# Kernel tuning notes

Measured on AMD Instinct MI355X. Metric: run time of the kernel, lower is better.

Reference implementation:

```python
import jax, jax.numpy as jnp
import numpy as np

H = 12      # num_heads
DIN = 768   # input_embedding_dim
D = 64      # embedding_dim (per head)
N, T = 4, 1024


def setup_inputs() -> dict:
    key = jax.random.key(0)
    ks = jax.random.split(key, 6)
    s_in = 1.0 / np.sqrt(DIN)
    s_hd = 1.0 / np.sqrt(H * D)
    x = jax.random.normal(ks[0], (N, T, DIN), dtype=jnp.float32)
    # Per-head bias-free projections stacked over heads: [H, DIN, D]
    Wq = jax.random.uniform(ks[1], (H, DIN, D), jnp.float32, -s_in, s_in)
    Wk = jax.random.uniform(ks[2], (H, DIN, D), jnp.float32, -s_in, s_in)
    Wv = jax.random.uniform(ks[3], (H, DIN, D), jnp.float32, -s_in, s_in)
    # Output projection: Linear(H*D -> D) with bias
    Wo = jax.random.uniform(ks[4], (H * D, D), jnp.float32, -s_hd, s_hd)
    bo = jax.random.uniform(ks[5], (D,), jnp.float32, -s_hd, s_hd)
    return {"x": x, "Wq": Wq, "Wk": Wk, "Wv": Wv, "Wo": Wo, "bo": bo}


def reference(x, Wq, Wk, Wv, Wo, bo):
    n, t, _ = x.shape
    # Batched per-head projections (all heads at once): [N,H,T,D]
    q = jnp.einsum('ntd,hde->nhte', x, Wq)
    k = jnp.einsum('ntd,hde->nhte', x, Wk)
    v = jnp.einsum('ntd,hde->nhte', x, Wv)
    # Raw scores (note: original applies NO 1/sqrt(D) scaling): [N,H,T,T]
    att = jnp.einsum('nhte,nhse->nhts', q, k)
    # Faithful to torch: tril zeros the upper triangle, then ALL zeros -> -inf
    causal = jnp.tril(jnp.ones((t, t), dtype=bool))
    att = jnp.where(causal, att, 0.0)
    att = jnp.where(att == 0.0, -jnp.inf, att)
    attn = jax.nn.softmax(att, axis=-1)  # [N,H,T,T]
    # Weighted values, then concat heads along feature dim (head-major order)
    o = jnp.einsum('nhts,nhse->nhte', attn, v)          # [N,H,T,D]
    o = jnp.transpose(o, (0, 2, 1, 3)).reshape(n, t, -1)  # [N,T,H*D]
    out = o @ Wo + bo  # [N,T,D]
    return out, attn
```

## Files before the change

kernel.cpp:

```cpp
#include <hip/hip_runtime.h>
#include <hip/hip_bf16.h>

typedef __hip_bfloat16 bf16;
typedef __attribute__((ext_vector_type(8))) short bf16x8;
typedef __attribute__((ext_vector_type(4))) float f32x4;

constexpr int NB  = 4;
constexpr int NH  = 12;
constexpr int SEQ = 1024;
constexpr int HD  = 64;
constexpr int DM  = 768;
constexpr int LDA = 40;

__device__ __forceinline__ bf16x8 ld8(const bf16* p){ return *(const bf16x8*)p; }
__device__ __forceinline__ f32x4 mfma16(bf16x8 a, bf16x8 b, f32x4 c){
  return __builtin_amdgcn_mfma_f32_16x16x32_bf16(a, b, c, 0, 0, 0);
}
union U8 { bf16x8 v; bf16 h[8]; };

__global__ __launch_bounds__(256) void wprep(const float* __restrict__ Wq, const float* __restrict__ Wk,
                      const float* __restrict__ Wv, const float* __restrict__ Wo,
                      bf16* __restrict__ WqTh, bf16* __restrict__ WqTl,
                      bf16* __restrict__ WkTh, bf16* __restrict__ WkTl,
                      bf16* __restrict__ WvT,  bf16* __restrict__ WoT){
  __shared__ float sT[64][65];
  const int tid = threadIdx.x;
  const int dt = blockIdx.x, y = blockIdx.y;
  const float* src; bf16* dh; bf16* dl = nullptr;
  if (y < 36){
    int z = y / 12, h = y % 12;
    src = (z==0 ? Wq : z==1 ? Wk : Wv) + (size_t)h*DM*HD;
    dh  = (z==0 ? WqTh : z==1 ? WkTh : WvT) + (size_t)h*HD*DM;
    if (z==0) dl = WqTl + (size_t)h*HD*DM;
    if (z==1) dl = WkTl + (size_t)h*HD*DM;
  } else { src = Wo; dh = WoT; }

  {
    int r = tid >> 2, c = (tid & 3) * 16;
    const float* sp = src + ((size_t)(dt*64 + r))*HD + c;
    f32x4 v0 = *(const f32x4*)sp, v1 = *(const f32x4*)(sp+4),
          v2 = *(const f32x4*)(sp+8), v3 = *(const f32x4*)(sp+12);
    #pragma unroll
    for (int j = 0; j < 4; j++){
      sT[r][c+j] = v0[j]; sT[r][c+4+j] = v1[j]; sT[r][c+8+j] = v2[j]; sT[r][c+12+j] = v3[j];
    }
  }
  __syncthreads();
  {
    int e = tid >> 2, co = (tid & 3) * 16;
    U8 uh0, ul0, uh1, ul1;
    #pragma unroll
    for (int j = 0; j < 8; j++){
      float v = sT[co + j][e];
      bf16 hi = __float2bfloat16(v);
      uh0.h[j] = hi; ul0.h[j] = __float2bfloat16(v - __bfloat162float(hi));
    }
    #pragma unroll
    for (int j = 0; j < 8; j++){
      float v = sT[co + 8 + j][e];
      bf16 hi = __float2bfloat16(v);
      uh1.h[j] = hi; ul1.h[j] = __float2bfloat16(v - __bfloat162float(hi));
    }
    size_t o = (size_t)e*DM + dt*64 + co;
    *(bf16x8*)(dh + o) = uh0.v; *(bf16x8*)(dh + o + 8) = uh1.v;
    if (dl){ *(bf16x8*)(dl + o) = ul0.v; *(bf16x8*)(dl + o + 8) = ul1.v; }
  }
}

__global__ __launch_bounds__(256) void xprep(const float* __restrict__ x,
                                             bf16* __restrict__ xh, bf16* __restrict__ xl){
  size_t base = ((size_t)blockIdx.x*256 + threadIdx.x)*8;
  f32x4 a = *(const f32x4*)(x + base), b = *(const f32x4*)(x + base + 4);
  U8 uh, ul;
  #pragma unroll
  for (int j = 0; j < 4; j++){
    bf16 h0 = __float2bfloat16(a[j]);
    uh.h[j] = h0; ul.h[j] = __float2bfloat16(a[j] - __bfloat162float(h0));
    bf16 h1 = __float2bfloat16(b[j]);
    uh.h[4+j] = h1; ul.h[4+j] = __float2bfloat16(b[j] - __bfloat162float(h1));
  }
  *(bf16x8*)(xh + base) = uh.v;
  *(bf16x8*)(xl + base) = ul.v;
}

__global__ __launch_bounds__(256) void kproj(const bf16* __restrict__ xh, const bf16* __restrict__ xl,
    const bf16* __restrict__ WqTh, const bf16* __restrict__ WqTl,
    const bf16* __restrict__ WkTh, const bf16* __restrict__ WkTl,
    const bf16* __restrict__ WvT,
    bf16* __restrict__ Qhi, bf16* __restrict__ Qlo,
    bf16* __restrict__ Khi, bf16* __restrict__ Klo, bf16* __restrict__ Vt){
  __shared__ bf16 sA[2][128*LDA];
  __shared__ bf16 sB[4][64*LDA];
  const int tid = threadIdx.x;
  const int lane = tid & 63, w = tid >> 6;
  const int quad = lane >> 4, lc = lane & 15;
  const int mb = blockIdx.x, h = blockIdx.y, z = blockIdx.z;
  const int sr = tid >> 2;
  const int sc = (tid & 3) * 8;
  const int wm = w & 1, wn = w >> 1;

  if (z == 0){
    const bf16* Bqh = WqTh + (size_t)h*HD*DM;
    const bf16* Bql = WqTl + (size_t)h*HD*DM;
    const bf16* Bkh = WkTh + (size_t)h*HD*DM;
    const bf16* Bkl = WkTl + (size_t)h*HD*DM;
    f32x4 aq[4][2] = {}, ak[4][2] = {};
    bf16x8 pa0,pa1,pa2,pa3,pq0,pq1,pk0,pk1;
    auto ldchunk = [&](int kc){
      size_t col = (size_t)kc*32 + sc;
      pa0 = ld8(xh + (size_t)(mb*128 + sr)*DM + col);
      pa1 = ld8(xh + (size_t)(mb*128 + sr + 64)*DM + col);
      pa2 = ld8(xl + (size_t)(mb*128 + sr)*DM + col);
      pa3 = ld8(xl + (size_t)(mb*128 + sr + 64)*DM + col);
      pq0 = ld8(Bqh + (size_t)sr*DM + col);
      pq1 = ld8(Bql + (size_t)sr*DM + col);
      pk0 = ld8(Bkh + (size_t)sr*DM + col);
      pk1 = ld8(Bkl + (size_t)sr*DM + col);
    };
    ldchunk(0);
    for (int kc = 0; kc < DM/32; kc++){
      *(bf16x8*)&sA[0][sr*LDA + sc] = pa0;
      *(bf16x8*)&sA[0][(sr+64)*LDA + sc] = pa1;
      *(bf16x8*)&sA[1][sr*LDA + sc] = pa2;
      *(bf16x8*)&sA[1][(sr+64)*LDA + sc] = pa3;
      *(bf16x8*)&sB[0][sr*LDA + sc] = pq0;
      *(bf16x8*)&sB[1][sr*LDA + sc] = pq1;
      *(bf16x8*)&sB[2][sr*LDA + sc] = pk0;
      *(bf16x8*)&sB[3][sr*LDA + sc] = pk1;
      __syncthreads();
      if (kc < DM/32 - 1) ldchunk(kc + 1);
      bf16x8 bqh[2], bql[2], bkh[2], bkl[2];
      #pragma unroll
      for (int nt = 0; nt < 2; nt++){
        int ro = (wn*32 + nt*16 + lc)*LDA + quad*8;
        bqh[nt] = *(const bf16x8*)&sB[0][ro];
        bql[nt] = *(const bf16x8*)&sB[1][ro];
        bkh[nt] = *(const bf16x8*)&sB[2][ro];
        bkl[nt] = *(const bf16x8*)&sB[3][ro];
      }
      #pragma unroll
      for (int mt = 0; mt < 4; mt++){
        bf16x8 ah = *(const bf16x8*)&sA[0][(wm*64 + mt*16 + lc)*LDA + quad*8];
        bf16x8 al = *(const bf16x8*)&sA[1][(wm*64 + mt*16 + lc)*LDA + quad*8];
        #pragma unroll
        for (int nt = 0; nt < 2; nt++){
          aq[mt][nt] = mfma16(ah, bqh[nt], aq[mt][nt]);
          aq[mt][nt] = mfma16(ah, bql[nt], aq[mt][nt]);
          aq[mt][nt] = mfma16(al, bqh[nt], aq[mt][nt]);
          ak[mt][nt] = mfma16(ah, bkh[nt], ak[mt][nt]);
          ak[mt][nt] = mfma16(ah, bkl[nt], ak[mt][nt]);
          ak[mt][nt] = mfma16(al, bkh[nt], ak[mt][nt]);
        }
      }
      __syncthreads();
    }
    #pragma unroll
    for (int mt = 0; mt < 4; mt++){
      #pragma unroll
      for (int nt = 0; nt < 2; nt++){
        #pragma unroll
        for (int i = 0; i < 4; i++){
          int tg = mb*128 + wm*64 + mt*16 + quad*4 + i;
          int e  = wn*32 + nt*16 + lc;
          int n = tg >> 10, t = tg & 1023;
          size_t o = ((size_t)(n*NH + h)*SEQ + t)*HD + e;
          float vq = aq[mt][nt][i];
          bf16 hq = __float2bfloat16(vq);
          Qhi[o] = hq;
          Qlo[o] = __float2bfloat16(vq - __bfloat162float(hq));
          float vk = ak[mt][nt][i];
          bf16 hk = __float2bfloat16(vk);
          Khi[o] = hk;
          Klo[o] = __float2bfloat16(vk - __bfloat162float(hk));
        }
      }
    }
  } else {
    const bf16* Av = WvT + (size_t)h*HD*DM;
    f32x4 acc[2][4] = {};
    bf16x8 pa0, pb0, pb1;
    auto ldchunk = [&](int kc){
      size_t col = (size_t)kc*32 + sc;
      pa0 = ld8(Av + (size_t)sr*DM + col);
      pb0 = ld8(xh + (size_t)(mb*128 + sr)*DM + col);
      pb1 = ld8(xh + (size_t)(mb*128 + sr + 64)*DM + col);
    };
    ldchunk(0);
    for (int kc = 0; kc < DM/32; kc++){
      *(bf16x8*)&sB[0][sr*LDA + sc] = pa0;
      *(bf16x8*)&sA[0][sr*LDA + sc] = pb0;
      *(bf16x8*)&sA[0][(sr+64)*LDA + sc] = pb1;
      __syncthreads();
      if (kc < DM/32 - 1) ldchunk(kc + 1);
      bf16x8 bt[4];
      #pragma unroll
      for (int nt = 0; nt < 4; nt++)
        bt[nt] = *(const bf16x8*)&sA[0][(wn*64 + nt*16 + lc)*LDA + quad*8];
      #pragma unroll
      for (int mt = 0; mt < 2; mt++){
        bf16x8 a = *(const bf16x8*)&sB[0][(wm*32 + mt*16 + lc)*LDA + quad*8];
        #pragma unroll
        for (int nt = 0; nt < 4; nt++)
          acc[mt][nt] = mfma16(a, bt[nt], acc[mt][nt]);
      }
      __syncthreads();
    }
    #pragma unroll
    for (int mt = 0; mt < 2; mt++){
      #pragma unroll
      for (int nt = 0; nt < 4; nt++){
        #pragma unroll
        for (int i = 0; i < 4; i++){
          int e  = wm*32 + mt*16 + quad*4 + i;
          int tg = mb*128 + wn*64 + nt*16 + lc;
          int n = tg >> 10, t = tg & 1023;
          Vt[((size_t)(n*NH + h)*HD + e)*SEQ + t] = __float2bfloat16(acc[mt][nt][i]);
        }
      }
    }
  }
}

__global__ __launch_bounds__(256) void kattn_pv(const bf16* __restrict__ Qhi, const bf16* __restrict__ Qlo,
                                                const bf16* __restrict__ Khi, const bf16* __restrict__ Klo,
                                                const bf16* __restrict__ Vt,
                                                float* __restrict__ attn, bf16* __restrict__ O){
  __shared__ bf16 sP[16][SEQ + 8];
  __shared__ float msh[4][16], lsh[4][16];
  const int tid = threadIdx.x;
  const int lane = tid & 63, w = tid >> 6;
  const int quad = lane >> 4, lc = lane & 15;
  const int t0 = blockIdx.x * 16;
  const int nh = blockIdx.y;
  const size_t base = (size_t)nh * SEQ * HD;
  const float NEGINF = -__builtin_inff();

  f32x4 acc[16] = {};
  const bf16* qh = Qhi + base + (size_t)(t0 + lc)*HD;
  const bf16* ql = Qlo + base + (size_t)(t0 + lc)*HD;
  bf16x8 ah0 = ld8(qh + quad*8), ah1 = ld8(qh + 32 + quad*8);
  bf16x8 al0 = ld8(ql + quad*8), al1 = ld8(ql + 32 + quad*8);
  const int tmax = t0 + 15;
  const int cbase = w*256;

  bf16x8 kb[2][4];
  auto loadK = [&](int tl, int b){
    const bf16* kh = Khi + base + (size_t)(cbase + tl*16 + lc)*HD;
    const bf16* kl = Klo + base + (size_t)(cbase + tl*16 + lc)*HD;
    kb[b][0] = ld8(kh + quad*8);  kb[b][1] = ld8(kh + 32 + quad*8);
    kb[b][2] = ld8(kl + quad*8);  kb[b][3] = ld8(kl + 32 + quad*8);
  };
  if (cbase <= tmax) loadK(0, 0);
  #pragma unroll
  for (int tl = 0; tl < 16; tl++){
    if (cbase + tl*16 <= tmax){
      if (tl < 15 && cbase + (tl+1)*16 <= tmax) loadK(tl+1, (tl+1)&1);
      const int b = tl & 1;
      acc[tl] = mfma16(ah0, kb[b][0], acc[tl]);
      acc[tl] = mfma16(ah1, kb[b][1], acc[tl]);
      acc[tl] = mfma16(ah0, kb[b][2], acc[tl]);
      acc[tl] = mfma16(ah1, kb[b][3], acc[tl]);
      acc[tl] = mfma16(al0, kb[b][0], acc[tl]);
      acc[tl] = mfma16(al1, kb[b][1], acc[tl]);
    }
  }

  float mx[4] = {NEGINF, NEGINF, NEGINF, NEGINF};
  #pragma unroll
  for (int tl = 0; tl < 16; tl++){
    int col = cbase + tl*16 + lc;
    #pragma unroll
    for (int i = 0; i < 4; i++){
      int r = t0 + quad*4 + i;
      float v = acc[tl][i];
      if (col <= r && v != 0.0f) mx[i] = fmaxf(mx[i], v);
    }
  }
  #pragma unroll
  for (int off = 8; off; off >>= 1){
    #pragma unroll
    for (int i = 0; i < 4; i++) mx[i] = fmaxf(mx[i], __shfl_xor(mx[i], off, 16));
  }
  float sm[4] = {0.f, 0.f, 0.f, 0.f};
  #pragma unroll
  for (int tl = 0; tl < 16; tl++){
    int col = cbase + tl*16 + lc;
    #pragma unroll
    for (int i = 0; i < 4; i++){
      int r = t0 + quad*4 + i;
      float v = acc[tl][i];
      float e = (col <= r && v != 0.0f) ? __expf(v - mx[i]) : 0.0f;
      acc[tl][i] = e;
      sm[i] += e;
    }
  }
  #pragma unroll
  for (int off = 8; off; off >>= 1){
    #pragma unroll
    for (int i = 0; i < 4; i++) sm[i] += __shfl_xor(sm[i], off, 16);
  }
  if (lc == 0){
    #pragma unroll
    for (int i = 0; i < 4; i++){ msh[w][quad*4 + i] = mx[i]; lsh[w][quad*4 + i] = sm[i]; }
  }
  __syncthreads();
  float scale[4];
  #pragma unroll
  for (int i = 0; i < 4; i++){
    int rl = quad*4 + i;
    float M = fmaxf(fmaxf(msh[0][rl], msh[1][rl]), fmaxf(msh[2][rl], msh[3][rl]));
    float L = 0.f;
    #pragma unroll
    for (int w2 = 0; w2 < 4; w2++) L += lsh[w2][rl] * __expf(msh[w2][rl] - M);
    scale[i] = __expf(mx[i] - M) / L;
  }
  #pragma unroll
  for (int tl = 0; tl < 16; tl++){
    int col = cbase + tl*16 + lc;
    #pragma unroll
    for (int i = 0; i < 4; i++){
      sP[quad*4 + i][col] = __float2bfloat16(acc[tl][i] * scale[i]);
    }
  }
  __syncthreads();

  #pragma unroll
  for (int r = 0; r < 16; r++){
    const unsigned* sPu = (const unsigned*)&sP[r][0];
    uint2 v = *(const uint2*)(sPu + tid*2);
    f32x4 f;
    f[0] = __uint_as_float(v.x << 16);
    f[1] = __uint_as_float(v.x & 0xFFFF0000u);
    f[2] = __uint_as_float(v.y << 16);
    f[3] = __uint_as_float(v.y & 0xFFFF0000u);
    *(f32x4*)(attn + ((size_t)nh*SEQ + t0 + r)*SEQ + tid*4) = f;
  }

  f32x4 oacc = {};
  const bf16* Vb = Vt + ((size_t)nh*HD + w*16 + lc)*SEQ;
  const int kend = t0 + 16;
  for (int s0 = 0; s0 < kend; s0 += 32){
    bf16x8 a = *(const bf16x8*)&sP[lc][s0 + quad*8];
    bf16x8 b = ld8(Vb + s0 + quad*8);
    oacc = mfma16(a, b, oacc);
  }
  const int n = nh / NH, h = nh % NH;
  #pragma unroll
  for (int i = 0; i < 4; i++){
    O[((size_t)n*SEQ + t0 + quad*4 + i)*DM + h*HD + w*16 + lc] = __float2bfloat16(oacc[i]);
  }
}

__global__ __launch_bounds__(256) void kout(const bf16* __restrict__ O, const bf16* __restrict__ WoT,
                                            const float* __restrict__ bo, float* __restrict__ out){
  const int lane = threadIdx.x & 63, w = threadIdx.x >> 6;
  const int quad = lane >> 4, lc = lane & 15;
  const int wm = w & 1, wn = w >> 1;
  const int g = blockIdx.x * 32;
  const int n = g >> 10, tb = g & 1023;
  const bf16* Or = O + ((size_t)n*SEQ + tb + wm*16 + lc)*DM;
  f32x4 acc[2] = {};
  for (int k0 = 0; k0 < DM; k0 += 32){
    bf16x8 a = ld8(Or + k0 + quad*8);
    #pragma unroll
    for (int nt = 0; nt < 2; nt++){
      bf16x8 b = ld8(WoT + (size_t)(wn*32 + nt*16 + lc)*DM + k0 + quad*8);
      acc[nt] = mfma16(a, b, acc[nt]);
    }
  }
  #pragma unroll
  for (int nt = 0; nt < 2; nt++){
    float bias = bo[wn*32 + nt*16 + lc];
    #pragma unroll
    for (int i = 0; i < 4; i++){
      out[((size_t)n*SEQ + tb + wm*16 + quad*4 + i)*HD + wn*32 + nt*16 + lc] = acc[nt][i] + bias;
    }
  }
}

extern "C" void kernel_launch(void* const* d_in, const int* in_sizes, int n_in,
                              void* d_out, int out_size, void* d_ws, size_t ws_size,
                              hipStream_t stream){
  const float* x  = (const float*)d_in[0];
  const float* Wq = (const float*)d_in[1];
  const float* Wk = (const float*)d_in[2];
  const float* Wv = (const float*)d_in[3];
  const float* Wo = (const float*)d_in[4];
  const float* bo = (const float*)d_in[5];

  float* out  = (float*)d_out;
  float* attn = out + (size_t)NB*SEQ*HD;

  constexpr size_t SZ_WT  = (size_t)NH*HD*DM;
  constexpr size_t SZ_WOT = (size_t)HD*DM;
  constexpr size_t SZ_Q   = (size_t)NB*NH*SEQ*HD;
  bf16* b = (bf16*)d_ws;
  bf16* WqTh = b;  b += SZ_WT;
  bf16* WqTl = b;  b += SZ_WT;
  bf16* WkTh = b;  b += SZ_WT;
  bf16* WkTl = b;  b += SZ_WT;
  bf16* WvT  = b;  b += SZ_WT;
  bf16* WoT  = b;  b += SZ_WOT;
  bf16* xh   = b;  b += SZ_Q;
  bf16* xl   = b;  b += SZ_Q;
  bf16* Qhi  = b;  b += SZ_Q;
  bf16* Qlo  = b;  b += SZ_Q;
  bf16* Khi  = b;  b += SZ_Q;
  bf16* Klo  = b;  b += SZ_Q;
  bf16* Vt   = b;  b += SZ_Q;
  bf16* O    = xh;

  wprep<<<dim3(12, 37), 256, 0, stream>>>(Wq, Wk, Wv, Wo, WqTh, WqTl, WkTh, WkTl, WvT, WoT);
  xprep<<<dim3((int)(SZ_Q/(256*8))), 256, 0, stream>>>(x, xh, xl);
  kproj<<<dim3(NB*SEQ/128, NH, 2), 256, 0, stream>>>(xh, xl, WqTh, WqTl, WkTh, WkTl, WvT,
                                                     Qhi, Qlo, Khi, Klo, Vt);
  kattn_pv<<<dim3(SEQ/16, NB*NH), 256, 0, stream>>>(Qhi, Qlo, Khi, Klo, Vt, attn, O);
  kout<<<dim3(NB*SEQ/32), 256, 0, stream>>>(O, WoT, bo, out);
}
```

Before: 366.3 us.

## Balance causal tiles across waves, remap blocks per XCD, stream attn stores

```diff
diff --git a/kernel.cpp b/kernel.cpp
--- a/kernel.cpp
+++ b/kernel.cpp
@@ -230,31 +230,40 @@
   const int tid = threadIdx.x;
   const int lane = tid & 63, w = tid >> 6;
   const int quad = lane >> 4, lc = lane & 15;
-  const int t0 = blockIdx.x * 16;
-  const int nh = blockIdx.y;
+  const int lin = blockIdx.x;
+  const int xcd = lin & 7;
+  const int c   = lin >> 3;
+  const int nh  = xcd * 6 + (c >> 6);
+  const int tt  = c & 63;
+  const int t0  = tt * 16;
   const size_t base = (size_t)nh * SEQ * HD;
   const float NEGINF = -__builtin_inff();
+
+  const int kend = t0 + 16;
+  const int T_act = tt + 1;
+  const int cnt   = (T_act + 3) >> 2;
+  const int wbase = w * cnt;
+  int wtiles = T_act - wbase;
+  wtiles = wtiles < 0 ? 0 : (wtiles > cnt ? cnt : wtiles);
 
   f32x4 acc[16] = {};
   const bf16* qh = Qhi + base + (size_t)(t0 + lc)*HD;
   const bf16* ql = Qlo + base + (size_t)(t0 + lc)*HD;
   bf16x8 ah0 = ld8(qh + quad*8), ah1 = ld8(qh + 32 + quad*8);
   bf16x8 al0 = ld8(ql + quad*8), al1 = ld8(ql + 32 + quad*8);
-  const int tmax = t0 + 15;
-  const int cbase = w*256;
 
   bf16x8 kb[2][4];
   auto loadK = [&](int tl, int b){
-    const bf16* kh = Khi + base + (size_t)(cbase + tl*16 + lc)*HD;
-    const bf16* kl = Klo + base + (size_t)(cbase + tl*16 + lc)*HD;
+    const bf16* kh = Khi + base + (size_t)((wbase + tl)*16 + lc)*HD;
+    const bf16* kl = Klo + base + (size_t)((wbase + tl)*16 + lc)*HD;
     kb[b][0] = ld8(kh + quad*8);  kb[b][1] = ld8(kh + 32 + quad*8);
     kb[b][2] = ld8(kl + quad*8);  kb[b][3] = ld8(kl + 32 + quad*8);
   };
-  if (cbase <= tmax) loadK(0, 0);
+  if (wtiles > 0) loadK(0, 0);
   #pragma unroll
   for (int tl = 0; tl < 16; tl++){
-    if (cbase + tl*16 <= tmax){
-      if (tl < 15 && cbase + (tl+1)*16 <= tmax) loadK(tl+1, (tl+1)&1);
+    if (tl < wtiles){
+      if (tl + 1 < wtiles) loadK(tl + 1, (tl + 1) & 1);
       const int b = tl & 1;
       acc[tl] = mfma16(ah0, kb[b][0], acc[tl]);
       acc[tl] = mfma16(ah1, kb[b][1], acc[tl]);
@@ -268,12 +277,14 @@
   float mx[4] = {NEGINF, NEGINF, NEGINF, NEGINF};
   #pragma unroll
   for (int tl = 0; tl < 16; tl++){
-    int col = cbase + tl*16 + lc;
-    #pragma unroll
-    for (int i = 0; i < 4; i++){
-      int r = t0 + quad*4 + i;
-      float v = acc[tl][i];
-      if (col <= r && v != 0.0f) mx[i] = fmaxf(mx[i], v);
+    if (tl < wtiles){
+      int col = (wbase + tl)*16 + lc;
+      #pragma unroll
+      for (int i = 0; i < 4; i++){
+        int r = t0 + quad*4 + i;
+        float v = acc[tl][i];
+        if (col <= r && v != 0.0f) mx[i] = fmaxf(mx[i], v);
+      }
     }
   }
   #pragma unroll
@@ -284,14 +295,16 @@
   float sm[4] = {0.f, 0.f, 0.f, 0.f};
   #pragma unroll
   for (int tl = 0; tl < 16; tl++){
-    int col = cbase + tl*16 + lc;
-    #pragma unroll
-    for (int i = 0; i < 4; i++){
-      int r = t0 + quad*4 + i;
-      float v = acc[tl][i];
-      float e = (col <= r && v != 0.0f) ? __expf(v - mx[i]) : 0.0f;
-      acc[tl][i] = e;
-      sm[i] += e;
+    if (tl < wtiles){
+      int col = (wbase + tl)*16 + lc;
+      #pragma unroll
+      for (int i = 0; i < 4; i++){
+        int r = t0 + quad*4 + i;
+        float v = acc[tl][i];
+        float e = (col <= r && v != 0.0f) ? __expf(v - mx[i]) : 0.0f;
+        acc[tl][i] = e;
+        sm[i] += e;
+      }
     }
   }
   #pragma unroll
@@ -316,33 +329,44 @@
   }
   #pragma unroll
   for (int tl = 0; tl < 16; tl++){
-    int col = cbase + tl*16 + lc;
-    #pragma unroll
-    for (int i = 0; i < 4; i++){
-      sP[quad*4 + i][col] = __float2bfloat16(acc[tl][i] * scale[i]);
-    }
+    if (tl < wtiles){
+      int col = (wbase + tl)*16 + lc;
+      #pragma unroll
+      for (int i = 0; i < 4; i++){
+        sP[quad*4 + i][col] = __float2bfloat16(acc[tl][i] * scale[i]);
+      }
+    }
+  }
+  if (kend & 31){
+    sP[tid >> 4][kend + (tid & 15)] = __float2bfloat16(0.0f);
   }
   __syncthreads();
 
   #pragma unroll
   for (int r = 0; r < 16; r++){
-    const unsigned* sPu = (const unsigned*)&sP[r][0];
-    uint2 v = *(const uint2*)(sPu + tid*2);
     f32x4 f;
-    f[0] = __uint_as_float(v.x << 16);
-    f[1] = __uint_as_float(v.x & 0xFFFF0000u);
-    f[2] = __uint_as_float(v.y << 16);
-    f[3] = __uint_as_float(v.y & 0xFFFF0000u);
-    *(f32x4*)(attn + ((size_t)nh*SEQ + t0 + r)*SEQ + tid*4) = f;
+    const int colb = tid * 4;
+    if (colb < kend){
+      const unsigned* sPu = (const unsigned*)&sP[r][0];
+      uint2 v = *(const uint2*)(sPu + tid*2);
+      f[0] = __uint_as_float(v.x << 16);
+      f[1] = __uint_as_float(v.x & 0xFFFF0000u);
+      f[2] = __uint_as_float(v.y << 16);
+      f[3] = __uint_as_float(v.y & 0xFFFF0000u);
+    } else {
+      f[0] = 0.f; f[1] = 0.f; f[2] = 0.f; f[3] = 0.f;
+    }
+    __builtin_nontemporal_store(f, (f32x4*)(attn + ((size_t)nh*SEQ + t0 + r)*SEQ + colb));
   }
 
   f32x4 oacc = {};
   const bf16* Vb = Vt + ((size_t)nh*HD + w*16 + lc)*SEQ;
-  const int kend = t0 + 16;
+  bf16x8 vnext = ld8(Vb + quad*8);
   for (int s0 = 0; s0 < kend; s0 += 32){
+    bf16x8 vcur = vnext;
+    if (s0 + 32 < kend) vnext = ld8(Vb + s0 + 32 + quad*8);
     bf16x8 a = *(const bf16x8*)&sP[lc][s0 + quad*8];
-    bf16x8 b = ld8(Vb + s0 + quad*8);
-    oacc = mfma16(a, b, oacc);
+    oacc = mfma16(a, vcur, oacc);
   }
   const int n = nh / NH, h = nh % NH;
   #pragma unroll
@@ -355,26 +379,20 @@
                                             const float* __restrict__ bo, float* __restrict__ out){
   const int lane = threadIdx.x & 63, w = threadIdx.x >> 6;
   const int quad = lane >> 4, lc = lane & 15;
-  const int wm = w & 1, wn = w >> 1;
-  const int g = blockIdx.x * 32;
+  const int g = blockIdx.x * 16;
   const int n = g >> 10, tb = g & 1023;
-  const bf16* Or = O + ((size_t)n*SEQ + tb + wm*16 + lc)*DM;
-  f32x4 acc[2] = {};
+  const bf16* Or = O + ((size_t)n*SEQ + tb + lc)*DM;
+  const bf16* Wr = WoT + (size_t)(w*16 + lc)*DM;
+  f32x4 acc = {};
   for (int k0 = 0; k0 < DM; k0 += 32){
     bf16x8 a = ld8(Or + k0 + quad*8);
-    #pragma unroll
-    for (int nt = 0; nt < 2; nt++){
-      bf16x8 b = ld8(WoT + (size_t)(wn*32 + nt*16 + lc)*DM + k0 + quad*8);
-      acc[nt] = mfma16(a, b, acc[nt]);
-    }
-  }
-  #pragma unroll
-  for (int nt = 0; nt < 2; nt++){
-    float bias = bo[wn*32 + nt*16 + lc];
-    #pragma unroll
-    for (int i = 0; i < 4; i++){
-      out[((size_t)n*SEQ + tb + wm*16 + quad*4 + i)*HD + wn*32 + nt*16 + lc] = acc[nt][i] + bias;
-    }
+    bf16x8 b = ld8(Wr + k0 + quad*8);
+    acc = mfma16(a, b, acc);
+  }
+  float bias = bo[w*16 + lc];
+  #pragma unroll
+  for (int i = 0; i < 4; i++){
+    out[((size_t)n*SEQ + tb + quad*4 + i)*HD + w*16 + lc] = acc[i] + bias;
   }
 }
 
@@ -414,6 +432,6 @@
   xprep<<<dim3((int)(SZ_Q/(256*8))), 256, 0, stream>>>(x, xh, xl);
   kproj<<<dim3(NB*SEQ/128, NH, 2), 256, 0, stream>>>(xh, xl, WqTh, WqTl, WkTh, WkTl, WvT,
                                                      Qhi, Qlo, Khi, Klo, Vt);
-  kattn_pv<<<dim3(SEQ/16, NB*NH), 256, 0, stream>>>(Qhi, Qlo, Khi, Klo, Vt, attn, O);
-  kout<<<dim3(NB*SEQ/32), 256, 0, stream>>>(O, WoT, bo, out);
-}
+  kattn_pv<<<dim3(NB*NH*SEQ/16), 256, 0, stream>>>(Qhi, Qlo, Khi, Klo, Vt, attn, O);
+  kout<<<dim3(NB*SEQ/16), 256, 0, stream>>>(O, WoT, bo, out);
+}
```

Measured after the change: 344.9 us. -5.8%, faster.
